# Kernel optimization log

Measured on AMD Instinct MI355X. Metric: run time of the kernel, lower is better.

## Reference

```python
import jax, jax.numpy as jnp
import numpy as np
import math

NUM_HEADS = 8


def _skew(QEr):
    # QEr: (B, H, S, S). Music-Transformer skew: pad one col on the left,
    # reshape (S, S+1) -> (S+1, S), drop first row -> relative scores Srel.
    B, H, S, _ = QEr.shape
    padded = jnp.pad(QEr, ((0, 0), (0, 0), (0, 0), (1, 0)))  # (B,H,S,S+1)
    reshaped = padded.reshape(B, H, S + 1, S)
    return reshaped[:, :, 1:, :]  # (B,H,S,S)


def setup_inputs() -> dict:
    key = jax.random.key(0)
    ks = jax.random.split(key, 8)
    B, S, D = 4, 2048, 512
    dh = D // NUM_HEADS
    scale = 0.02
    return {
        "x": jax.random.normal(ks[0], (B, S, D), jnp.float32),
        "Wq": jax.random.normal(ks[1], (D, D), jnp.float32) * scale,
        "bq": jnp.zeros((D,), jnp.float32),
        "Wk": jax.random.normal(ks[2], (D, D), jnp.float32) * scale,
        "bk": jnp.zeros((D,), jnp.float32),
        "Wv": jax.random.normal(ks[3], (D, D), jnp.float32) * scale,
        "bv": jnp.zeros((D,), jnp.float32),
        "Er": jax.random.normal(ks[4], (S, dh), jnp.float32),  # max_len == S
    }


def reference(x, Wq, bq, Wk, bk, Wv, bv, Er):
    B, S, D = x.shape
    H = NUM_HEADS
    dh = D // H
    # torch Linear: y = x @ W.T + b
    q = (x @ Wq.T + bq).reshape(B, S, H, dh).transpose(0, 2, 1, 3)  # (B,H,S,dh)
    k = (x @ Wk.T + bk).reshape(B, S, H, dh).transpose(0, 2, 1, 3)
    v = (x @ Wv.T + bv).reshape(B, S, H, dh).transpose(0, 2, 1, 3)
    # relative position scores; start = max_len - seq_len = 0 here
    max_len = Er.shape[0]
    Er_used = Er[max_len - S:, :]  # (S, dh)
    QEr = jnp.einsum("bhsd,rd->bhsr", q, Er_used)  # (B,H,S,S)
    Srel = _skew(QEr)
    scores = (jnp.einsum("bhsd,bhtd->bhst", q, k) + Srel) / math.sqrt(dh)
    causal = jnp.tril(jnp.ones((S, S), bool))
    scores = jnp.where(causal, scores, -jnp.inf)
    attn = jax.nn.softmax(scores, axis=-1)
    out = jnp.einsum("bhst,bhtd->bhsd", attn, v)  # (B,H,S,dh)
    return out.transpose(0, 2, 1, 3).reshape(B, S, D)
```

## Files before the change

### kernel.cpp

```cpp
#include <hip/hip_runtime.h>
#include <hip/hip_bf16.h>

#define S_LEN 2048
#define NHEADS 8
#define DHEAD 64
#define NBATCH 4
#define DMODEL 512

typedef __attribute__((ext_vector_type(8))) short short8;
typedef __attribute__((ext_vector_type(4))) short short4v;
typedef __attribute__((ext_vector_type(4))) float f32x4;

__device__ __forceinline__ short f2bf(float f) {
    unsigned int u = __builtin_bit_cast(unsigned int, f);
    u = (u + 0x7fffu + ((u >> 16) & 1u)) >> 16;
    return (short)u;
}

__global__ __launch_bounds__(256) void er_convert(const float* __restrict__ er,
                                                  unsigned short* __restrict__ erb) {
    int i = (blockIdx.x * 256 + threadIdx.x) * 4;
    float4 v = *(const float4*)(er + i);
    short4v s;
    s[0] = f2bf(v.x); s[1] = f2bf(v.y); s[2] = f2bf(v.z); s[3] = f2bf(v.w);
    *(short4v*)(erb + i) = s;
}

__global__ __launch_bounds__(256) void conv_bf16(
    const float* __restrict__ x, const float* __restrict__ Wq,
    const float* __restrict__ Wk, const float* __restrict__ Wv,
    unsigned short* __restrict__ xb, unsigned short* __restrict__ wb)
{
    const int bid = blockIdx.x;
    const float* src;
    unsigned short* dst;
    int idx;
    if (bid < 4096) {
        src = x; dst = xb; idx = bid * 256 + threadIdx.x;
    } else {
        const int m = (bid - 4096) >> 8;
        src = (m == 0) ? Wq : (m == 1) ? Wk : Wv;
        dst = wb + m * (DMODEL * DMODEL);
        idx = ((bid - 4096) & 255) * 256 + threadIdx.x;
    }
    float4 v = *(const float4*)(src + idx * 4);
    short4v s;
    s[0] = f2bf(v.x); s[1] = f2bf(v.y); s[2] = f2bf(v.z); s[3] = f2bf(v.w);
    *(short4v*)(dst + idx * 4) = s;
}

__global__ __launch_bounds__(256) void qkv_gemm(
    const unsigned short* __restrict__ xb,
    const unsigned short* __restrict__ wb,
    const float* __restrict__ bq, const float* __restrict__ bk,
    const float* __restrict__ bv,
    unsigned short* __restrict__ qkv)
{
    __shared__ __align__(16) short smem[64 * 136];
    short* xt = smem;
    short* wt = smem + 128 * 40;
    const int tid = threadIdx.x;
    const int w = tid >> 6;
    const int l = tid & 63;
    const int lrow = l & 15, lgrp = l >> 4;
    const int m0 = blockIdx.x * 128;
    const int nb = blockIdx.y;
    const int mat = nb >> 3, hh = nb & 7;
    const unsigned short* wmat = wb + mat * (DMODEL * DMODEL);
    const float* bias = (mat == 0) ? bq : ((mat == 1) ? bk : bv);
    const int n0 = hh * 64;

    f32x4 acc[2][4];
    #pragma unroll
    for (int i = 0; i < 2; i++)
        #pragma unroll
        for (int j = 0; j < 4; j++) acc[i][j] = (f32x4)0.0f;

    const int xur = tid >> 2, xus = tid & 3;
    const int wur = tid >> 2, wus = tid & 3;

    for (int k0 = 0; k0 < DMODEL; k0 += 32) {
        short8 xa0 = *(const short8*)(xb + (size_t)(m0 + xur) * DMODEL + k0 + xus * 8);
        short8 xa1 = *(const short8*)(xb + (size_t)(m0 + xur + 64) * DMODEL + k0 + xus * 8);
        short8 wa  = *(const short8*)(wmat + (size_t)(n0 + wur) * DMODEL + k0 + wus * 8);
        *(short8*)(xt + xur * 40 + xus * 8)        = xa0;
        *(short8*)(xt + (xur + 64) * 40 + xus * 8) = xa1;
        *(short8*)(wt + wur * 40 + wus * 8)        = wa;
        __syncthreads();
        #pragma unroll
        for (int nc = 0; nc < 4; nc++) {
            short8 bfrag = *(const short8*)(wt + (nc * 16 + lrow) * 40 + lgrp * 8);
            #pragma unroll
            for (int mf = 0; mf < 2; mf++) {
                short8 afrag = *(const short8*)(xt + (w * 32 + mf * 16 + lrow) * 40 + lgrp * 8);
                acc[mf][nc] = __builtin_amdgcn_mfma_f32_16x16x32_bf16(afrag, bfrag, acc[mf][nc], 0, 0, 0);
            }
        }
        __syncthreads();
    }

    const int b  = m0 >> 11;
    const int s0 = m0 & (S_LEN - 1);
    if (mat == 2) {
        short* vl = smem;
        #pragma unroll
        for (int nc = 0; nc < 4; nc++) {
            const int d = nc * 16 + lrow;
            const float bias_v = bias[n0 + d];
            #pragma unroll
            for (int mf = 0; mf < 2; mf++)
                #pragma unroll
                for (int r = 0; r < 4; r++) {
                    const int sl = w * 32 + mf * 16 + lgrp * 4 + r;
                    vl[d * 136 + sl] = f2bf(acc[mf][nc][r] + bias_v);
                }
        }
        __syncthreads();
        unsigned short* ob = qkv + (((size_t)2 * NBATCH + b) * NHEADS + hh) * S_LEN * DHEAD;
        #pragma unroll
        for (int kch = 0; kch < 4; kch++) {
            const int c = kch * 256 + tid;
            const int d = c >> 4, seg = c & 15;
            short8 ch = *(const short8*)(vl + d * 136 + seg * 8);
            *(short8*)(ob + (size_t)d * S_LEN + s0 + seg * 8) = ch;
        }
    } else {
        const float oscale = (mat == 0) ? 0.18033688f : 1.0f;
        unsigned short* ob = qkv + (((size_t)mat * NBATCH + b) * NHEADS + hh) * S_LEN * DHEAD;
        #pragma unroll
        for (int nc = 0; nc < 4; nc++) {
            const int d = nc * 16 + lrow;
            const float bias_v = bias[n0 + d];
            #pragma unroll
            for (int mf = 0; mf < 2; mf++) {
                #pragma unroll
                for (int r = 0; r < 4; r++) {
                    int srow = s0 + w * 32 + mf * 16 + lgrp * 4 + r;
                    ob[(size_t)srow * DHEAD + d] =
                        (unsigned short)f2bf((acc[mf][nc][r] + bias_v) * oscale);
                }
            }
        }
    }
}

__global__ __launch_bounds__(256) void rga_attn(
    const unsigned short* __restrict__ qkv,
    const unsigned short* __restrict__ er,
    float* __restrict__ out)
{
    __shared__ __align__(16) unsigned short klds[2][64 * 64];
    __shared__ __align__(16) unsigned short vt[2][64 * 72];
    __shared__ __align__(16) unsigned short plds[4][16 * 64];

    const int tid = threadIdx.x;
    const int w = tid >> 6;
    const int l = tid & 63;
    const int lrow = l & 15, lgrp = l >> 4;
    const int p  = blockIdx.x;
    const int bh = blockIdx.y;
    const int b = bh >> 3, hh = bh & 7;

    const unsigned short* qp  = qkv + (size_t)bh * S_LEN * DHEAD;
    const unsigned short* kp  = qkv + ((size_t)(NBATCH * NHEADS) + bh) * S_LEN * DHEAD;
    const unsigned short* vtg = qkv + ((size_t)(2 * NBATCH * NHEADS) + bh) * S_LEN * DHEAD;

    short8 ones;
    #pragma unroll
    for (int e = 0; e < 8; e++) ones[e] = (short)0x3F80;

    const int tr0 = tid >> 3, tr1 = (tid >> 3) + 32, seg = tid & 7;
    unsigned short* pw = plds[w];

    #pragma unroll 1
    for (int sp = 0; sp < 2; sp++) {
        const int sid = sp ? p : (31 - p);
        const int q0 = sid * 64;
        const int s_base = q0 + w * 16;
        const int nt = sid + 1;

        short8 aq[2];
        {
            const unsigned short* qr = qp + (size_t)(s_base + lrow) * DHEAD + lgrp * 8;
            aq[0] = *(const short8*)(qr);
            aq[1] = *(const short8*)(qr + 32);
        }

        f32x4 o[4], lsum;
        lsum = (f32x4)0.0f;
        #pragma unroll
        for (int n = 0; n < 4; n++) o[n] = (f32x4)0.0f;

        short8 kreg[2], vreg[2], ereg0[5], ereg1[5];
        kreg[0] = *(const short8*)(kp + (size_t)tr0 * DHEAD + seg * 8);
        kreg[1] = *(const short8*)(kp + (size_t)tr1 * DHEAD + seg * 8);
        vreg[0] = *(const short8*)(vtg + (size_t)tr0 * S_LEN + seg * 8);
        vreg[1] = *(const short8*)(vtg + (size_t)tr1 * S_LEN + seg * 8);
        *(short8*)((char*)klds[0] + tr0 * 128 + ((seg * 16) ^ ((tr0 & 7) << 4))) = kreg[0];
        *(short8*)((char*)klds[0] + tr1 * 128 + ((seg * 16) ^ ((tr1 & 7) << 4))) = kreg[1];
        *(short8*)(vt[0] + tr0 * 72 + seg * 8) = vreg[0];
        *(short8*)(vt[0] + tr1 * 72 + seg * 8) = vreg[1];
        if (nt > 1) {
            kreg[0] = *(const short8*)(kp + (size_t)(64 + tr0) * DHEAD + seg * 8);
            kreg[1] = *(const short8*)(kp + (size_t)(64 + tr1) * DHEAD + seg * 8);
            vreg[0] = *(const short8*)(vtg + (size_t)tr0 * S_LEN + 64 + seg * 8);
            vreg[1] = *(const short8*)(vtg + (size_t)tr1 * S_LEN + 64 + seg * 8);
        }
        {
            const int r_lo = -s_base + (S_LEN - 16);
            #pragma unroll
            for (int f = 0; f < 5; f++) {
                int rr = r_lo + f * 16 + lrow;
                rr = rr < 0 ? 0 : (rr > (S_LEN - 1) ? (S_LEN - 1) : rr);
                const unsigned short* ep = er + (size_t)rr * DHEAD + lgrp * 8;
                ereg0[f] = *(const short8*)(ep);
                ereg1[f] = *(const short8*)(ep + 32);
            }
        }
        __syncthreads();

        for (int it = 0; it < nt; it++) {
            const int t0 = it << 6;
            const int cur = it & 1;
            if (it + 1 < nt) {
                unsigned short* kd = klds[cur ^ 1];
                unsigned short* vd = vt[cur ^ 1];
                *(short8*)((char*)kd + tr0 * 128 + ((seg * 16) ^ ((tr0 & 7) << 4))) = kreg[0];
                *(short8*)((char*)kd + tr1 * 128 + ((seg * 16) ^ ((tr1 & 7) << 4))) = kreg[1];
                *(short8*)(vd + tr0 * 72 + seg * 8) = vreg[0];
                *(short8*)(vd + tr1 * 72 + seg * 8) = vreg[1];
            }
            f32x4 qe[5];
            __builtin_amdgcn_s_setprio(1);
            #pragma unroll
            for (int f = 0; f < 5; f++) {
                f32x4 a = (f32x4)0.0f;
                a = __builtin_amdgcn_mfma_f32_16x16x32_bf16(aq[0], ereg0[f], a, 0, 0, 0);
                a = __builtin_amdgcn_mfma_f32_16x16x32_bf16(aq[1], ereg1[f], a, 0, 0, 0);
                qe[f] = a;
            }
            __builtin_amdgcn_s_setprio(0);
            if (it + 2 < nt) {
                const int tn = t0 + 128;
                kreg[0] = *(const short8*)(kp + (size_t)(tn + tr0) * DHEAD + seg * 8);
                kreg[1] = *(const short8*)(kp + (size_t)(tn + tr1) * DHEAD + seg * 8);
                vreg[0] = *(const short8*)(vtg + (size_t)tr0 * S_LEN + tn + seg * 8);
                vreg[1] = *(const short8*)(vtg + (size_t)tr1 * S_LEN + tn + seg * 8);
            }
            if (it + 1 < nt) {
                const int r_lo = t0 + 64 - s_base + (S_LEN - 16);
                #pragma unroll
                for (int f = 0; f < 5; f++) {
                    int rr = r_lo + f * 16 + lrow;
                    rr = rr < 0 ? 0 : (rr > (S_LEN - 1) ? (S_LEN - 1) : rr);
                    const unsigned short* ep = er + (size_t)rr * DHEAD + lgrp * 8;
                    ereg0[f] = *(const short8*)(ep);
                    ereg1[f] = *(const short8*)(ep + 32);
                }
            }
            f32x4 sfr[4];
            __builtin_amdgcn_s_setprio(1);
            #pragma unroll
            for (int u = 0; u < 4; u++) {
                const int trow = u * 16 + lrow;
                const char* kb = (const char*)klds[cur] + trow * 128;
                const int swz = (trow & 7) << 4;
                short8 kb0 = *(const short8*)(kb + ((lgrp * 16) ^ swz));
                short8 kb1 = *(const short8*)(kb + ((64 + lgrp * 16) ^ swz));
                f32x4 a = (f32x4)0.0f;
                a = __builtin_amdgcn_mfma_f32_16x16x32_bf16(aq[0], kb0, a, 0, 0, 0);
                a = __builtin_amdgcn_mfma_f32_16x16x32_bf16(aq[1], kb1, a, 0, 0, 0);
                sfr[u] = a;
            }
            __builtin_amdgcn_s_setprio(0);
            #pragma unroll
            for (int r = 0; r < 4; r++) {
                const int si = lgrp * 4 + r;
                const int sg = s_base + si;
                const int dd = lrow - si + 15;
                const int srcl = (l & 48) | (dd & 15);
                const int hi = dd >> 4;
                float sh[5];
                #pragma unroll
                for (int f = 0; f < 5; f++) sh[f] = __shfl(qe[f][r], srcl);
                const int pswz = (si & 7) << 4;
                char* pr = (char*)pw + si * 128;
                float pe[4];
                #pragma unroll
                for (int u = 0; u < 4; u++) {
                    const float rel = hi ? sh[u + 1] : sh[u];
                    float sc = sfr[u][r] + rel;
                    float ex;
                    asm("v_exp_f32 %0, %1\ns_nop 1" : "=v"(ex) : "v"(sc));
                    pe[u] = ((t0 + u * 16 + lrow) <= sg) ? ex : 0.0f;
                }
                #pragma unroll
                for (int h2 = 0; h2 < 2; h2++) {
                    unsigned pk;
                    asm("v_cvt_pk_bf16_f32 %0, %1, %2"
                        : "=v"(pk) : "v"(pe[h2 * 2]), "v"(pe[h2 * 2 + 1]));
                    *(unsigned short*)(pr + (((h2 * 32 + lrow) * 2) ^ pswz)) = (unsigned short)pk;
                    *(unsigned short*)(pr + (((h2 * 32 + 16 + lrow) * 2) ^ pswz)) = (unsigned short)(pk >> 16);
                }
            }
            asm volatile("s_waitcnt lgkmcnt(0)" ::: "memory");
            __builtin_amdgcn_sched_barrier(0);
            __builtin_amdgcn_s_setprio(1);
            const int pswz2 = (lrow & 7) << 4;
            #pragma unroll
            for (int kk = 0; kk < 2; kk++) {
                short8 pa = *(const short8*)((const char*)pw + lrow * 128 +
                                             ((kk * 64 + lgrp * 16) ^ pswz2));
                lsum = __builtin_amdgcn_mfma_f32_16x16x32_bf16(pa, ones, lsum, 0, 0, 0);
                #pragma unroll
                for (int n = 0; n < 4; n++) {
                    short8 vb = *(const short8*)(vt[cur] + (n * 16 + lrow) * 72 + kk * 32 + lgrp * 8);
                    o[n] = __builtin_amdgcn_mfma_f32_16x16x32_bf16(pa, vb, o[n], 0, 0, 0);
                }
            }
            __builtin_amdgcn_s_setprio(0);
            __syncthreads();
        }

        #pragma unroll
        for (int r = 0; r < 4; r++) {
            const int sg = s_base + lgrp * 4 + r;
            const float inv = 1.0f / lsum[r];
            float* orow = out + ((size_t)b * S_LEN + sg) * DMODEL + hh * DHEAD;
            #pragma unroll
            for (int n = 0; n < 4; n++)
                orow[n * 16 + lrow] = o[n][r] * inv;
        }
    }
}

extern "C" void kernel_launch(void* const* d_in, const int* in_sizes, int n_in,
                              void* d_out, int out_size, void* d_ws, size_t ws_size,
                              hipStream_t stream) {
    const float* x  = (const float*)d_in[0];
    const float* Wq = (const float*)d_in[1];
    const float* bq = (const float*)d_in[2];
    const float* Wk = (const float*)d_in[3];
    const float* bk = (const float*)d_in[4];
    const float* Wv = (const float*)d_in[5];
    const float* bv = (const float*)d_in[6];
    const float* Er = (const float*)d_in[7];

    unsigned short* ws_qkv = (unsigned short*)d_ws;
    unsigned short* ws_er  = ws_qkv + (size_t)3 * NBATCH * NHEADS * S_LEN * DHEAD;

    unsigned short* xb = (unsigned short*)d_out;
    unsigned short* wb = xb + (size_t)NBATCH * S_LEN * DMODEL;

    conv_bf16<<<dim3(4096 + 3 * 256), dim3(256), 0, stream>>>(x, Wq, Wk, Wv, xb, wb);
    er_convert<<<dim3(128), dim3(256), 0, stream>>>(Er, ws_er);
    qkv_gemm<<<dim3(64, 24), dim3(256), 0, stream>>>(xb, wb, bq, bk, bv, ws_qkv);
    rga_attn<<<dim3(16, 32), dim3(256), 0, stream>>>(ws_qkv, ws_er, (float*)d_out);
}
```

Baseline: 127.3 us.

## Shrink attention blocks to two waves, load V from global, fold Er conversion

```diff
diff --git a/kernel.cpp b/kernel.cpp
--- a/kernel.cpp
+++ b/kernel.cpp
@@ -17,19 +17,12 @@
     return (short)u;
 }
 
-__global__ __launch_bounds__(256) void er_convert(const float* __restrict__ er,
-                                                  unsigned short* __restrict__ erb) {
-    int i = (blockIdx.x * 256 + threadIdx.x) * 4;
-    float4 v = *(const float4*)(er + i);
-    short4v s;
-    s[0] = f2bf(v.x); s[1] = f2bf(v.y); s[2] = f2bf(v.z); s[3] = f2bf(v.w);
-    *(short4v*)(erb + i) = s;
-}
-
 __global__ __launch_bounds__(256) void conv_bf16(
     const float* __restrict__ x, const float* __restrict__ Wq,
     const float* __restrict__ Wk, const float* __restrict__ Wv,
-    unsigned short* __restrict__ xb, unsigned short* __restrict__ wb)
+    const float* __restrict__ er,
+    unsigned short* __restrict__ xb, unsigned short* __restrict__ wb,
+    unsigned short* __restrict__ erb)
 {
     const int bid = blockIdx.x;
     const float* src;
@@ -37,11 +30,14 @@
     int idx;
     if (bid < 4096) {
         src = x; dst = xb; idx = bid * 256 + threadIdx.x;
-    } else {
+    } else if (bid < 4864) {
         const int m = (bid - 4096) >> 8;
         src = (m == 0) ? Wq : (m == 1) ? Wk : Wv;
         dst = wb + m * (DMODEL * DMODEL);
         idx = ((bid - 4096) & 255) * 256 + threadIdx.x;
+    } else {
+        src = er; dst = erb;
+        idx = (bid - 4864) * 256 + threadIdx.x;
     }
     float4 v = *(const float4*)(src + idx * 4);
     short4v s;
@@ -144,20 +140,19 @@
     }
 }
 
-__global__ __launch_bounds__(256) void rga_attn(
+__global__ __launch_bounds__(128) void rga_attn(
     const unsigned short* __restrict__ qkv,
     const unsigned short* __restrict__ er,
     float* __restrict__ out)
 {
     __shared__ __align__(16) unsigned short klds[2][64 * 64];
-    __shared__ __align__(16) unsigned short vt[2][64 * 72];
-    __shared__ __align__(16) unsigned short plds[4][16 * 64];
+    __shared__ __align__(16) unsigned short plds[2][16 * 64];
 
     const int tid = threadIdx.x;
     const int w = tid >> 6;
     const int l = tid & 63;
     const int lrow = l & 15, lgrp = l >> 4;
-    const int p  = blockIdx.x;
+    const int j  = blockIdx.x;
     const int bh = blockIdx.y;
     const int b = bh >> 3, hh = bh & 7;
 
@@ -169,15 +164,15 @@
     #pragma unroll
     for (int e = 0; e < 8; e++) ones[e] = (short)0x3F80;
 
-    const int tr0 = tid >> 3, tr1 = (tid >> 3) + 32, seg = tid & 7;
+    const int trb = tid >> 3, seg = tid & 7;
     unsigned short* pw = plds[w];
 
     #pragma unroll 1
     for (int sp = 0; sp < 2; sp++) {
-        const int sid = sp ? p : (31 - p);
-        const int q0 = sid * 64;
+        const int ks = sp ? j : (63 - j);
+        const int q0 = ks * 32;
         const int s_base = q0 + w * 16;
-        const int nt = sid + 1;
+        const int nt = (ks >> 1) + 1;
 
         short8 aq[2];
         {
@@ -191,20 +186,19 @@
         #pragma unroll
         for (int n = 0; n < 4; n++) o[n] = (f32x4)0.0f;
 
-        short8 kreg[2], vreg[2], ereg0[5], ereg1[5];
-        kreg[0] = *(const short8*)(kp + (size_t)tr0 * DHEAD + seg * 8);
-        kreg[1] = *(const short8*)(kp + (size_t)tr1 * DHEAD + seg * 8);
-        vreg[0] = *(const short8*)(vtg + (size_t)tr0 * S_LEN + seg * 8);
-        vreg[1] = *(const short8*)(vtg + (size_t)tr1 * S_LEN + seg * 8);
-        *(short8*)((char*)klds[0] + tr0 * 128 + ((seg * 16) ^ ((tr0 & 7) << 4))) = kreg[0];
-        *(short8*)((char*)klds[0] + tr1 * 128 + ((seg * 16) ^ ((tr1 & 7) << 4))) = kreg[1];
-        *(short8*)(vt[0] + tr0 * 72 + seg * 8) = vreg[0];
-        *(short8*)(vt[0] + tr1 * 72 + seg * 8) = vreg[1];
+        short8 kreg[4], ereg0[5], ereg1[5];
+        #pragma unroll
+        for (int u = 0; u < 4; u++)
+            kreg[u] = *(const short8*)(kp + (size_t)(trb + 16 * u) * DHEAD + seg * 8);
+        #pragma unroll
+        for (int u = 0; u < 4; u++) {
+            const int tr = trb + 16 * u;
+            *(short8*)((char*)klds[0] + tr * 128 + ((seg * 16) ^ ((tr & 7) << 4))) = kreg[u];
+        }
         if (nt > 1) {
-            kreg[0] = *(const short8*)(kp + (size_t)(64 + tr0) * DHEAD + seg * 8);
-            kreg[1] = *(const short8*)(kp + (size_t)(64 + tr1) * DHEAD + seg * 8);
-            vreg[0] = *(const short8*)(vtg + (size_t)tr0 * S_LEN + 64 + seg * 8);
-            vreg[1] = *(const short8*)(vtg + (size_t)tr1 * S_LEN + 64 + seg * 8);
+            #pragma unroll
+            for (int u = 0; u < 4; u++)
+                kreg[u] = *(const short8*)(kp + (size_t)(64 + trb + 16 * u) * DHEAD + seg * 8);
         }
         {
             const int r_lo = -s_base + (S_LEN - 16);
@@ -224,11 +218,11 @@
             const int cur = it & 1;
             if (it + 1 < nt) {
                 unsigned short* kd = klds[cur ^ 1];
-                unsigned short* vd = vt[cur ^ 1];
-                *(short8*)((char*)kd + tr0 * 128 + ((seg * 16) ^ ((tr0 & 7) << 4))) = kreg[0];
-                *(short8*)((char*)kd + tr1 * 128 + ((seg * 16) ^ ((tr1 & 7) << 4))) = kreg[1];
-                *(short8*)(vd + tr0 * 72 + seg * 8) = vreg[0];
-                *(short8*)(vd + tr1 * 72 + seg * 8) = vreg[1];
+                #pragma unroll
+                for (int u = 0; u < 4; u++) {
+                    const int tr = trb + 16 * u;
+                    *(short8*)((char*)kd + tr * 128 + ((seg * 16) ^ ((tr & 7) << 4))) = kreg[u];
+                }
             }
             f32x4 qe[5];
             __builtin_amdgcn_s_setprio(1);
@@ -242,10 +236,9 @@
             __builtin_amdgcn_s_setprio(0);
             if (it + 2 < nt) {
                 const int tn = t0 + 128;
-                kreg[0] = *(const short8*)(kp + (size_t)(tn + tr0) * DHEAD + seg * 8);
-                kreg[1] = *(const short8*)(kp + (size_t)(tn + tr1) * DHEAD + seg * 8);
-                vreg[0] = *(const short8*)(vtg + (size_t)tr0 * S_LEN + tn + seg * 8);
-                vreg[1] = *(const short8*)(vtg + (size_t)tr1 * S_LEN + tn + seg * 8);
+                #pragma unroll
+                for (int u = 0; u < 4; u++)
+                    kreg[u] = *(const short8*)(kp + (size_t)(tn + trb + 16 * u) * DHEAD + seg * 8);
             }
             if (it + 1 < nt) {
                 const int r_lo = t0 + 64 - s_base + (S_LEN - 16);
@@ -273,6 +266,13 @@
                 sfr[u] = a;
             }
             __builtin_amdgcn_s_setprio(0);
+            short8 vb[2][4];
+            #pragma unroll
+            for (int kk = 0; kk < 2; kk++)
+                #pragma unroll
+                for (int n = 0; n < 4; n++)
+                    vb[kk][n] = *(const short8*)(vtg + (size_t)(n * 16 + lrow) * S_LEN
+                                                 + t0 + kk * 32 + lgrp * 8);
             #pragma unroll
             for (int r = 0; r < 4; r++) {
                 const int si = lgrp * 4 + r;
@@ -313,10 +313,8 @@
                                              ((kk * 64 + lgrp * 16) ^ pswz2));
                 lsum = __builtin_amdgcn_mfma_f32_16x16x32_bf16(pa, ones, lsum, 0, 0, 0);
                 #pragma unroll
-                for (int n = 0; n < 4; n++) {
-                    short8 vb = *(const short8*)(vt[cur] + (n * 16 + lrow) * 72 + kk * 32 + lgrp * 8);
-                    o[n] = __builtin_amdgcn_mfma_f32_16x16x32_bf16(pa, vb, o[n], 0, 0, 0);
-                }
+                for (int n = 0; n < 4; n++)
+                    o[n] = __builtin_amdgcn_mfma_f32_16x16x32_bf16(pa, vb[kk][n], o[n], 0, 0, 0);
             }
             __builtin_amdgcn_s_setprio(0);
             __syncthreads();
@@ -352,8 +350,7 @@
     unsigned short* xb = (unsigned short*)d_out;
     unsigned short* wb = xb + (size_t)NBATCH * S_LEN * DMODEL;
 
-    conv_bf16<<<dim3(4096 + 3 * 256), dim3(256), 0, stream>>>(x, Wq, Wk, Wv, xb, wb);
-    er_convert<<<dim3(128), dim3(256), 0, stream>>>(Er, ws_er);
+    conv_bf16<<<dim3(4096 + 3 * 256 + 128), dim3(256), 0, stream>>>(x, Wq, Wk, Wv, Er, xb, wb, ws_er);
     qkv_gemm<<<dim3(64, 24), dim3(256), 0, stream>>>(xb, wb, bq, bk, bv, ws_qkv);
-    rga_attn<<<dim3(16, 32), dim3(256), 0, stream>>>(ws_qkv, ws_er, (float*)d_out);
-}
+    rga_attn<<<dim3(32, 32), dim3(128), 0, stream>>>(ws_qkv, ws_er, (float*)d_out);
+}
```

Result: slower. 177.1 us (+39.1%).
